# Optimization experiments

Measured on AMD Instinct MI355X. Metric: run time of the kernel, lower is better.

The kernel has to match this reference:

```python
import jax, jax.numpy as jnp
import numpy as np
from jax import lax

V = 37        # 3 special tokens + 34 Georgian letters
E = 256       # embed_dim
H = 1024      # hidden_dim
B = 2048      # batch
S = 24        # src len
T = 24        # tgt len (= max_len)
SOS = 1       # index of '<SOS>' in vocab


def _lstm_layer(x, h0, c0, W_ih, W_hh, b_ih, b_hh):
    """Single PyTorch-style LSTM layer. x: [B,S,D_in] -> (ys [B,S,H], hN, cN).
    Gate order i, f, g, o as in torch.nn.LSTM."""
    xg = jnp.einsum('bsd,gd->bsg', x, W_ih) + b_ih  # [B,S,4H], input projection precomputed

    def step(carry, xg_t):
        h, c = carry
        gates = xg_t + h @ W_hh.T + b_hh            # [B,4H]
        i, f, g, o = jnp.split(gates, 4, axis=-1)
        i = jax.nn.sigmoid(i)
        f = jax.nn.sigmoid(f)
        g = jnp.tanh(g)
        o = jax.nn.sigmoid(o)
        c = f * c + i * g
        h = o * jnp.tanh(c)
        return (h, c), h

    (hN, cN), ys = lax.scan(step, (h0, c0), jnp.swapaxes(xg, 0, 1))  # scan over time
    return jnp.swapaxes(ys, 0, 1), hN, cN


def _lstm2(x, h0s, c0s, p0, p1):
    """2-layer stacked LSTM (dropout inactive in eval). h0s/c0s: tuples per layer."""
    y0, h0N, c0N = _lstm_layer(x, h0s[0], c0s[0], *p0)
    y1, h1N, c1N = _lstm_layer(y0, h0s[1], c0s[1], *p1)
    return y1, (h0N, h1N), (c0N, c1N)


def setup_inputs() -> dict:
    key = jax.random.key(0)
    ks = jax.random.split(key, 24)

    def p(k, shape, scale=0.05):
        return (jax.random.normal(k, shape) * scale).astype(jnp.float32)

    inp = {
        'src': jax.random.randint(ks[0], (B, S), 0, V),
        'tgt': jax.random.randint(ks[1], (B, T), 0, V),
        'emb': p(ks[2], (V, E)),
        # encoder layer 0 / 1
        'eW_ih0': p(ks[3], (4 * H, E)), 'eW_hh0': p(ks[4], (4 * H, H)),
        'eb_ih0': p(ks[5], (4 * H,)),   'eb_hh0': p(ks[6], (4 * H,)),
        'eW_ih1': p(ks[7], (4 * H, H)), 'eW_hh1': p(ks[8], (4 * H, H)),
        'eb_ih1': p(ks[9], (4 * H,)),   'eb_hh1': p(ks[10], (4 * H,)),
        # decoder layer 0 / 1
        'dW_ih0': p(ks[11], (4 * H, E)), 'dW_hh0': p(ks[12], (4 * H, H)),
        'db_ih0': p(ks[13], (4 * H,)),   'db_hh0': p(ks[14], (4 * H,)),
        'dW_ih1': p(ks[15], (4 * H, H)), 'dW_hh1': p(ks[16], (4 * H, H)),
        'db_ih1': p(ks[17], (4 * H,)),   'db_hh1': p(ks[18], (4 * H,)),
        # output projection
        'fcW': p(ks[19], (V, H)), 'fcb': p(ks[20], (V,)),
    }
    return inp


def reference(src, tgt, emb,
              eW_ih0, eW_hh0, eb_ih0, eb_hh0, eW_ih1, eW_hh1, eb_ih1, eb_hh1,
              dW_ih0, dW_hh0, db_ih0, db_hh0, dW_ih1, dW_hh1, db_ih1, db_hh1,
              fcW, fcb):
    dtype = emb.dtype
    z = jnp.zeros((src.shape[0], H), dtype)

    # --- encoder: consume src, keep final (h, c) per layer ---
    x_src = emb[src]                                          # [B,S,E]
    _, h_enc, c_enc = _lstm2(x_src, (z, z), (z, z),
                             (eW_ih0, eW_hh0, eb_ih0, eb_hh0),
                             (eW_ih1, eW_hh1, eb_ih1, eb_hh1))

    # --- decoder with full teacher forcing: inputs = [SOS, tgt[:, :-1]] ---
    sos = jnp.full((tgt.shape[0], 1), SOS, dtype=tgt.dtype)
    dec_tokens = jnp.concatenate([sos, tgt[:, :-1]], axis=1)  # [B,T]
    x_dec = emb[dec_tokens]                                   # [B,T,E]
    y, _, _ = _lstm2(x_dec, h_enc, c_enc,
                     (dW_ih0, dW_hh0, db_ih0, db_hh0),
                     (dW_ih1, dW_hh1, db_ih1, db_hh1))        # [B,T,H]

    logits = jnp.einsum('bth,vh->btv', y, fcW) + fcb          # [B,T,V]
    return logits
```

## Files before the change

kernel.cpp:

```cpp
#include <hip/hip_runtime.h>

typedef __attribute__((ext_vector_type(8))) short short8;
typedef __attribute__((ext_vector_type(4))) float floatx4;

#define BB 2048
#define SS 24
#define HH 1024
#define VV 37
#define EE 256
#define G4H 4096
#define OSTR (SS * VV)

__device__ __forceinline__ unsigned short f2bf(float f) {
    union { float f; unsigned u; } x; x.f = f;
    unsigned r = x.u + 0x7FFF + ((x.u >> 16) & 1);
    return (unsigned short)(r >> 16);
}
__device__ __forceinline__ float bf2f(unsigned short s) {
    union { unsigned u; float f; } x; x.u = ((unsigned)s) << 16; return x.f;
}
__device__ __forceinline__ float sigm(float x) {
    x = fminf(fmaxf(x, -15.f), 15.f);
    return 1.f / (1.f + __expf(-x));
}
__device__ __forceinline__ float tanh_(float x) {
    x = fminf(fmaxf(x, -15.f), 15.f);
    float e = __expf(2.f * x);
    return (e - 1.f) / (e + 1.f);
}

__device__ __forceinline__ int wrow_orig(int C) {
    return (((C >> 4) & 3) << 10) | ((C >> 6) << 4) | (C & 15);
}

typedef const __attribute__((address_space(1))) void* gas_t;
typedef __attribute__((address_space(3))) void* las_t;
__device__ __forceinline__ void gl_lds16(const void* g, void* l) {
    __builtin_amdgcn_global_load_lds((gas_t)g, (las_t)l, 16, 0, 0);
}

__global__ __launch_bounds__(256)
void cvt_pack_kernel(const float* __restrict__ s, unsigned short* __restrict__ d) {
    int g = blockIdx.x * 256 + threadIdx.x;
    int l   = g & 63;
    int blk = g >> 6;
    int kb  = blk & 31;
    int ct  = blk >> 5;
    int col = (ct << 4) + (l & 15);
    int k0  = (kb << 5) + ((l >> 4) << 3);
    const float* sp = s + (size_t)wrow_orig(col) * 1024 + k0;
    float4 v0 = *reinterpret_cast<const float4*>(sp);
    float4 v1 = *reinterpret_cast<const float4*>(sp + 4);
    ushort4 o0, o1;
    o0.x = f2bf(v0.x); o0.y = f2bf(v0.y); o0.z = f2bf(v0.z); o0.w = f2bf(v0.w);
    o1.x = f2bf(v1.x); o1.y = f2bf(v1.y); o1.z = f2bf(v1.z); o1.w = f2bf(v1.w);
    reinterpret_cast<ushort4*>(d)[(size_t)g * 2]     = o0;
    reinterpret_cast<ushort4*>(d)[(size_t)g * 2 + 1] = o1;
}

__global__ __launch_bounds__(256)
void cvt_fcw_kernel(const float* __restrict__ s, unsigned short* __restrict__ d) {
    int g = blockIdx.x * 256 + threadIdx.x;
    if (g >= 6144) return;
    int l   = g & 63;
    int blk = g >> 6;
    int kb  = blk & 31;
    int ct  = blk >> 5;
    int col = (ct << 4) + (l & 15);
    int k0  = (kb << 5) + ((l >> 4) << 3);
    ushort4 o0 = {0, 0, 0, 0}, o1 = {0, 0, 0, 0};
    if (col < VV) {
        const float* sp = s + (size_t)col * HH + k0;
        float4 v0 = *reinterpret_cast<const float4*>(sp);
        float4 v1 = *reinterpret_cast<const float4*>(sp + 4);
        o0.x = f2bf(v0.x); o0.y = f2bf(v0.y); o0.z = f2bf(v0.z); o0.w = f2bf(v0.w);
        o1.x = f2bf(v1.x); o1.y = f2bf(v1.y); o1.z = f2bf(v1.z); o1.w = f2bf(v1.w);
    }
    reinterpret_cast<ushort4*>(d)[(size_t)g * 2]     = o0;
    reinterpret_cast<ushort4*>(d)[(size_t)g * 2 + 1] = o1;
}

__global__ __launch_bounds__(256)
void out_init_kernel(const float* __restrict__ fcb, float* __restrict__ out, int n) {
    int i = blockIdx.x * 256 + threadIdx.x;
    if (i >= n) return;
    out[i] = fcb[i % VV];
}

__global__ __launch_bounds__(256) void zero16_kernel(uint4* __restrict__ p) {
    uint4 z; z.x = 0; z.y = 0; z.z = 0; z.w = 0;
    p[(size_t)blockIdx.x * 256 + threadIdx.x] = z;
}

__global__ __launch_bounds__(256)
void tok_kernel(const int* __restrict__ src, const int* __restrict__ tgt, int* __restrict__ toks) {
    int idx = blockIdx.x * 256 + threadIdx.x;
    int b  = idx & 2047;
    int st = idx >> 11;
    int tok;
    if (st < SS) tok = src[b * SS + st];
    else { int t = st - SS; tok = (t == 0) ? 1 : tgt[b * SS + (t - 1)]; }
    toks[idx] = tok;
}

__global__ __launch_bounds__(256) void bias_sum_kernel(
        const float* e0i, const float* e0h, const float* e1i, const float* e1h,
        const float* d0i, const float* d0h, const float* d1i, const float* d1h,
        float* __restrict__ out) {
    int idx = blockIdx.x * 256 + threadIdx.x;
    int layer = idx >> 12, C = idx & 4095;
    int src_j = wrow_orig(C);
    const float* pi; const float* ph;
    switch (layer) {
        case 0:  pi = e0i; ph = e0h; break;
        case 1:  pi = e1i; ph = e1h; break;
        case 2:  pi = d0i; ph = d0h; break;
        default: pi = d1i; ph = d1h; break;
    }
    out[idx] = pi[src_j] + ph[src_j];
}

__global__ __launch_bounds__(256)
void proj_kernel(const float* __restrict__ emb, const float* __restrict__ eWih,
                 const float* __restrict__ dWih, float* __restrict__ proj) {
    int bid = blockIdx.x;
    int table = bid / (VV * 16);
    int rem   = bid - table * (VV * 16);
    int v     = rem >> 4;
    int cblk  = rem & 15;
    const float* W = table ? dWih : eWih;
    __shared__ float es[EE];
    es[threadIdx.x] = emb[v * EE + threadIdx.x];
    __syncthreads();
    int C = (cblk << 8) + threadIdx.x;
    const float* wr = W + (size_t)wrow_orig(C) * EE;
    float acc = 0.f;
#pragma unroll 8
    for (int k = 0; k < EE; ++k) acc += es[k] * wr[k];
    proj[((size_t)table * VV + v) * G4H + C] = acc;
}

__global__ __launch_bounds__(256, 2)
void lstm_step(const unsigned short* __restrict__ A0, const unsigned short* __restrict__ W0,
               const unsigned short* __restrict__ A1, const unsigned short* __restrict__ W1,
               int nchunk,
               const float* __restrict__ bias, const float* __restrict__ prj,
               const int* __restrict__ tok,
               float* __restrict__ cst, unsigned short* __restrict__ hout)
{
    __shared__ __align__(16) unsigned short As[16384];
    __shared__ __align__(16) unsigned short Bs[16384];

    const int tid  = threadIdx.x;
    const int lane = tid & 63;
    const int wave = tid >> 6;
    const int wm = wave >> 1, wn = wave & 1;
    const int m0 = blockIdx.y << 7;
    const int n0 = blockIdx.x << 7;

    const int r16 = lane & 15;
    const int rtb = m0 >> 4;
    const int ctb = n0 >> 4;
    const size_t wlane = (size_t)(lane << 3);

    floatx4 acc[4][4];
#pragma unroll
    for (int i = 0; i < 4; ++i)
#pragma unroll
        for (int j = 0; j < 4; ++j)
            acc[i][j] = (floatx4){0.f, 0.f, 0.f, 0.f};

    for (int t = 0; t < nchunk; ++t) {
        const unsigned short* Ap = (t & 8) ? A1 : A0;
        const unsigned short* Wp = (t & 8) ? W1 : W0;
        const int kb0 = (t & 7) << 2;
#pragma unroll
        for (int kc = 0; kc < 4; ++kc) {
            gl_lds16(Ap + (((size_t)((rtb + wave) << 5) + kb0 + kc) << 9) + wlane,
                     As + (wave << 11) + (kc << 9));
            gl_lds16(Ap + (((size_t)((rtb + wave + 4) << 5) + kb0 + kc) << 9) + wlane,
                     As + ((wave + 4) << 11) + (kc << 9));
            gl_lds16(Wp + (((size_t)((ctb + wave) << 5) + kb0 + kc) << 9) + wlane,
                     Bs + (wave << 11) + (kc << 9));
            gl_lds16(Wp + (((size_t)((ctb + wave + 4) << 5) + kb0 + kc) << 9) + wlane,
                     Bs + ((wave + 4) << 11) + (kc << 9));
        }
        __syncthreads();

#pragma unroll
        for (int kc = 0; kc < 4; ++kc) {
            short8 af[4], bfr[4];
#pragma unroll
            for (int i = 0; i < 4; ++i) {
                af[i]  = *reinterpret_cast<const short8*>(As + ((((wm << 2) + i) << 11) + (kc << 9) + (lane << 3)));
                bfr[i] = *reinterpret_cast<const short8*>(Bs + ((((wn << 2) + i) << 11) + (kc << 9) + (lane << 3)));
            }
#pragma unroll
            for (int i = 0; i < 4; ++i)
#pragma unroll
                for (int j = 0; j < 4; ++j)
                    acc[i][j] = __builtin_amdgcn_mfma_f32_16x16x32_bf16(af[i], bfr[j], acc[i][j], 0, 0, 0);
        }
        __syncthreads();
    }

    const int q = lane >> 4;
    const int ub = (((n0 >> 6) + wn) << 4) + r16;
    float bj[4];
#pragma unroll
    for (int j = 0; j < 4; ++j)
        bj[j] = bias[n0 + (wn << 6) + (j << 4) + r16];

    const int kbu = ub >> 5;
    const int lq  = ((ub & 31) >> 3) << 4;
    const int eu  = ub & 7;

#pragma unroll
    for (int i = 0; i < 4; ++i) {
#pragma unroll
        for (int p = 0; p < 4; ++p) {
            const int row = m0 + (wm << 6) + (i << 4) + (q << 2) + p;
            float g0 = acc[i][0][p] + bj[0];
            float g1 = acc[i][1][p] + bj[1];
            float g2 = acc[i][2][p] + bj[2];
            float g3 = acc[i][3][p] + bj[3];
            if (prj != nullptr) {
                const float* pr = prj + (size_t)tok[row] * G4H + n0 + (wn << 6) + r16;
                g0 += pr[0]; g1 += pr[16]; g2 += pr[32]; g3 += pr[48];
            }
            const float iv = sigm(g0);
            const float fv = sigm(g1);
            const float gv = tanh_(g2);
            const float ov = sigm(g3);
            const size_t ci = (size_t)row * HH + ub;
            const float cc = fv * cst[ci] + iv * gv;
            cst[ci] = cc;
            const size_t hi = ((((size_t)((row >> 4) << 5) + kbu) << 6) + lq + (q << 2) + p) * 8 + eu;
            hout[hi] = f2bf(ov * tanh_(cc));
        }
    }
}

__global__ __launch_bounds__(256, 2)
void fc_mfma_kernel(const unsigned short* __restrict__ h1p, const unsigned short* __restrict__ fcWp,
                    float* __restrict__ out, int t) {
    __shared__ __align__(16) unsigned short As[16384];
    __shared__ __align__(16) unsigned short Bs[6144];

    const int lane = threadIdx.x & 63;
    const int wave = threadIdx.x >> 6;
    const int ks = blockIdx.x;
    const int mb = blockIdx.y;
    const int rtb = mb << 3;
    const int kb0 = ks << 2;
    const size_t wlane = (size_t)(lane << 3);

#pragma unroll
    for (int kc = 0; kc < 4; ++kc) {
        gl_lds16(h1p + (((size_t)((rtb + wave) << 5) + kb0 + kc) << 9) + wlane,
                 As + (wave << 11) + (kc << 9));
        gl_lds16(h1p + (((size_t)((rtb + wave + 4) << 5) + kb0 + kc) << 9) + wlane,
                 As + ((wave + 4) << 11) + (kc << 9));
    }
    if (wave < 3) {
#pragma unroll
        for (int kc = 0; kc < 4; ++kc)
            gl_lds16(fcWp + (((size_t)(wave << 5) + kb0 + kc) << 9) + wlane,
                     Bs + (wave << 11) + (kc << 9));
    }
    __syncthreads();

    floatx4 acc[2][3];
#pragma unroll
    for (int i = 0; i < 2; ++i)
#pragma unroll
        for (int j = 0; j < 3; ++j)
            acc[i][j] = (floatx4){0.f, 0.f, 0.f, 0.f};

#pragma unroll
    for (int kc = 0; kc < 4; ++kc) {
        short8 af[2], bfr[3];
        af[0] = *reinterpret_cast<const short8*>(As + ((wave << 11) + (kc << 9) + (lane << 3)));
        af[1] = *reinterpret_cast<const short8*>(As + (((wave + 4) << 11) + (kc << 9) + (lane << 3)));
#pragma unroll
        for (int j = 0; j < 3; ++j)
            bfr[j] = *reinterpret_cast<const short8*>(Bs + ((j << 11) + (kc << 9) + (lane << 3)));
#pragma unroll
        for (int i = 0; i < 2; ++i)
#pragma unroll
            for (int j = 0; j < 3; ++j)
                acc[i][j] = __builtin_amdgcn_mfma_f32_16x16x32_bf16(af[i], bfr[j], acc[i][j], 0, 0, 0);
    }

    const int r16 = lane & 15, q = lane >> 4;
#pragma unroll
    for (int j = 0; j < 3; ++j) {
        const int col = (j << 4) + r16;
        if (col < VV) {
#pragma unroll
            for (int i = 0; i < 2; ++i) {
#pragma unroll
                for (int p = 0; p < 4; ++p) {
                    const int row = (mb << 7) + ((wave + (i << 2)) << 4) + (q << 2) + p;
                    atomicAdd(out + (size_t)row * OSTR + t * VV + col, acc[i][j][p]);
                }
            }
        }
    }
}

extern "C" void kernel_launch(void* const* d_in, const int* in_sizes, int n_in,
                              void* d_out, int out_size, void* d_ws, size_t ws_size,
                              hipStream_t stream) {
    const int*   src    = (const int*)d_in[0];
    const int*   tgt    = (const int*)d_in[1];
    const float* emb    = (const float*)d_in[2];
    const float* eW_ih0 = (const float*)d_in[3];
    const float* eW_hh0 = (const float*)d_in[4];
    const float* eb_ih0 = (const float*)d_in[5];
    const float* eb_hh0 = (const float*)d_in[6];
    const float* eW_ih1 = (const float*)d_in[7];
    const float* eW_hh1 = (const float*)d_in[8];
    const float* eb_ih1 = (const float*)d_in[9];
    const float* eb_hh1 = (const float*)d_in[10];
    const float* dW_ih0 = (const float*)d_in[11];
    const float* dW_hh0 = (const float*)d_in[12];
    const float* db_ih0 = (const float*)d_in[13];
    const float* db_hh0 = (const float*)d_in[14];
    const float* dW_ih1 = (const float*)d_in[15];
    const float* dW_hh1 = (const float*)d_in[16];
    const float* db_ih1 = (const float*)d_in[17];
    const float* db_hh1 = (const float*)d_in[18];
    const float* fcW    = (const float*)d_in[19];
    const float* fcb    = (const float*)d_in[20];
    float* out = (float*)d_out;

    char* w = (char*)d_ws;
    size_t off = 0;
    auto walloc = [&](size_t bytes) { void* p = w + off; off += (bytes + 255) & ~(size_t)255; return p; };
    unsigned short* bW[8];
    const float* srcW[8] = {eW_ih0, eW_hh0, eW_ih1, eW_hh1, dW_ih0, dW_hh0, dW_ih1, dW_hh1};
    const int     szW[8] = {G4H*EE, G4H*HH, G4H*HH, G4H*HH, G4H*EE, G4H*HH, G4H*HH, G4H*HH};
    for (int i = 0; i < 8; ++i) bW[i] = (unsigned short*)walloc((size_t)szW[i] * 2);
    unsigned short* bfcWp = (unsigned short*)walloc((size_t)48 * HH * 2);
    unsigned short* h0a = (unsigned short*)walloc((size_t)BB * HH * 2);
    unsigned short* h1a = (unsigned short*)walloc((size_t)BB * HH * 2);
    float* c0 = (float*)walloc((size_t)BB * HH * 4);
    float* c1 = (float*)walloc((size_t)BB * HH * 4);
    unsigned short* h0b = (unsigned short*)walloc((size_t)BB * HH * 2);
    unsigned short* h1b = (unsigned short*)walloc((size_t)BB * HH * 2);
    float* bsum = (float*)walloc((size_t)4 * G4H * 4);
    int*   toks = (int*)walloc((size_t)2 * SS * BB * 4);
    float* proj = (float*)walloc((size_t)2 * VV * G4H * 4);

    unsigned short* h0[2] = {h0a, h0b};
    unsigned short* h1[2] = {h1a, h1b};

    for (int i = 0; i < 8; ++i) {
        if (i == 0 || i == 4) continue;
        cvt_pack_kernel<<<2048, 256, 0, stream>>>(srcW[i], bW[i]);
    }
    cvt_fcw_kernel<<<24, 256, 0, stream>>>(fcW, bfcWp);
    out_init_kernel<<<(BB * OSTR + 255) / 256, 256, 0, stream>>>(fcb, out, BB * OSTR);
    zero16_kernel<<<6144, 256, 0, stream>>>((uint4*)h0a);
    bias_sum_kernel<<<64, 256, 0, stream>>>(eb_ih0, eb_hh0, eb_ih1, eb_hh1,
                                            db_ih0, db_hh0, db_ih1, db_hh1, bsum);
    tok_kernel<<<384, 256, 0, stream>>>(src, tgt, toks);
    proj_kernel<<<2 * VV * 16, 256, 0, stream>>>(emb, eW_ih0, dW_ih0, proj);

    dim3 ggrid(G4H / 128, BB / 128);
    dim3 fgrid(8, 16);

    int p = 0;
    for (int t = 0; t < 2 * SS; ++t) {
        const int enc = (t < SS);
        const unsigned short* Whh0 = enc ? bW[1] : bW[5];
        const unsigned short* Whh1 = enc ? bW[3] : bW[7];
        const unsigned short* Wih1 = enc ? bW[2] : bW[6];
        const float* b0 = bsum + (size_t)(enc ? 0 : 2) * G4H;
        const float* b1 = bsum + (size_t)(enc ? 1 : 3) * G4H;
        const float* pj = proj + (size_t)(enc ? 0 : 1) * VV * G4H;

        lstm_step<<<ggrid, 256, 0, stream>>>(
            h0[p], Whh0, h0[p], Whh0, 8, b0, pj, toks + (size_t)t * BB, c0, h0[p ^ 1]);
        lstm_step<<<ggrid, 256, 0, stream>>>(
            h1[p], Whh1, h0[p ^ 1], Wih1, 16, b1, nullptr, nullptr, c1, h1[p ^ 1]);
        if (!enc)
            fc_mfma_kernel<<<fgrid, 256, 0, stream>>>(h1[p ^ 1], bfcWp, out, t - SS);
        p ^= 1;
    }
}
```

Measured before the change: 3.638 ms.

## Double-buffer LDS tiles in LSTM step GEMM to overlap loads with MFMA

```diff
diff --git a/kernel.cpp b/kernel.cpp
--- a/kernel.cpp
+++ b/kernel.cpp
@@ -140,7 +140,7 @@
     proj[((size_t)table * VV + v) * G4H + C] = acc;
 }
 
-__global__ __launch_bounds__(256, 2)
+__global__ __launch_bounds__(256, 1)
 void lstm_step(const unsigned short* __restrict__ A0, const unsigned short* __restrict__ W0,
                const unsigned short* __restrict__ A1, const unsigned short* __restrict__ W1,
                int nchunk,
@@ -148,8 +148,8 @@
                const int* __restrict__ tok,
                float* __restrict__ cst, unsigned short* __restrict__ hout)
 {
-    __shared__ __align__(16) unsigned short As[16384];
-    __shared__ __align__(16) unsigned short Bs[16384];
+    __shared__ __align__(16) unsigned short As[2][16384];
+    __shared__ __align__(16) unsigned short Bs[2][16384];
 
     const int tid  = threadIdx.x;
     const int lane = tid & 63;
@@ -170,30 +170,40 @@
         for (int j = 0; j < 4; ++j)
             acc[i][j] = (floatx4){0.f, 0.f, 0.f, 0.f};
 
-    for (int t = 0; t < nchunk; ++t) {
-        const unsigned short* Ap = (t & 8) ? A1 : A0;
-        const unsigned short* Wp = (t & 8) ? W1 : W0;
-        const int kb0 = (t & 7) << 2;
+    auto stage = [&](int c) {
+        const unsigned short* Ap = (c & 8) ? A1 : A0;
+        const unsigned short* Wp = (c & 8) ? W1 : W0;
+        const int kb0 = (c & 7) << 2;
+        unsigned short* Ad = As[c & 1];
+        unsigned short* Bd = Bs[c & 1];
 #pragma unroll
         for (int kc = 0; kc < 4; ++kc) {
             gl_lds16(Ap + (((size_t)((rtb + wave) << 5) + kb0 + kc) << 9) + wlane,
-                     As + (wave << 11) + (kc << 9));
+                     Ad + (wave << 11) + (kc << 9));
             gl_lds16(Ap + (((size_t)((rtb + wave + 4) << 5) + kb0 + kc) << 9) + wlane,
-                     As + ((wave + 4) << 11) + (kc << 9));
+                     Ad + ((wave + 4) << 11) + (kc << 9));
             gl_lds16(Wp + (((size_t)((ctb + wave) << 5) + kb0 + kc) << 9) + wlane,
-                     Bs + (wave << 11) + (kc << 9));
+                     Bd + (wave << 11) + (kc << 9));
             gl_lds16(Wp + (((size_t)((ctb + wave + 4) << 5) + kb0 + kc) << 9) + wlane,
-                     Bs + ((wave + 4) << 11) + (kc << 9));
+                     Bd + ((wave + 4) << 11) + (kc << 9));
         }
-        __syncthreads();
-
+    };
+
+    stage(0);
+    __syncthreads();
+
+#pragma unroll 1
+    for (int t = 0; t < nchunk; ++t) {
+        if (t + 1 < nchunk) stage(t + 1);
+        const unsigned short* Al = As[t & 1];
+        const unsigned short* Bl = Bs[t & 1];
 #pragma unroll
         for (int kc = 0; kc < 4; ++kc) {
             short8 af[4], bfr[4];
 #pragma unroll
             for (int i = 0; i < 4; ++i) {
-                af[i]  = *reinterpret_cast<const short8*>(As + ((((wm << 2) + i) << 11) + (kc << 9) + (lane << 3)));
-                bfr[i] = *reinterpret_cast<const short8*>(Bs + ((((wn << 2) + i) << 11) + (kc << 9) + (lane << 3)));
+                af[i]  = *reinterpret_cast<const short8*>(Al + ((((wm << 2) + i) << 11) + (kc << 9) + (lane << 3)));
+                bfr[i] = *reinterpret_cast<const short8*>(Bl + ((((wn << 2) + i) << 11) + (kc << 9) + (lane << 3)));
             }
 #pragma unroll
             for (int i = 0; i < 4; ++i)
```

After: 5.236 ms. 43.9% more time.
